# Optimization experiments

Hardware: AMD Instinct MI355X
Metric: run time of the kernel (lower is better)

## Reference

```python
import jax, jax.numpy as jnp
import numpy as np

HC, WC = 248, 224          # coarse grid
HF, WF = 496, 448
C, UNITS = 128, 256
U = UNITS // 4             # combination='concat' -> per-quadrant units


def _build_edges():
    """Upsampling edges: each fine node connects to its unique coarse parent.
    Quadrant split follows the original rel_pos conditions
    [(-0.5,0.5),(0.5,0.5),(0.5,-0.5),(-0.5,-0.5)] == (row,col) parity
    (even,odd),(odd,odd),(odd,even),(even,even)."""
    n_coarse = HC * WC
    rr, cc = np.meshgrid(np.arange(HF), np.arange(WF), indexing='ij')
    parent = (rr // 2) * WC + cc // 2                 # sender = coarse node id
    recv = n_coarse + rr * WF + cc                    # receiver = offset fine node id
    re, ce = rr % 2, cc % 2
    masks = [(re == 0) & (ce == 1), (re == 1) & (ce == 1),
             (re == 1) & (ce == 0), (re == 0) & (ce == 0)]
    return np.stack([np.stack([parent[m], recv[m]], -1) for m in masks]).astype(np.int32)


def setup_inputs() -> dict:
    key = jax.random.key(0)
    k = jax.random.split(key, 4)
    n_coarse = HC * WC
    return {
        'x': jax.random.normal(k[0], (n_coarse, C), jnp.float32),
        'W_emb': jax.random.normal(k[1], (4, C, U), jnp.float32) * 0.05,
        'W_edge': jax.random.normal(k[2], (4, 2 + 2 * U, U), jnp.float32) * 0.05,
        'W_node': jax.random.normal(k[3], (C + 4 * U, UNITS), jnp.float32) * 0.05,
        'edge_idx': jnp.asarray(_build_edges()),   # [4, E, 2] int32
    }


def reference(x, W_emb, W_edge, W_node, edge_idx):
    n_coarse = x.shape[0]
    n_fine = edge_idx.shape[0] * edge_idx.shape[1]
    n_total = n_coarse + n_fine
    # x = concat(old nodes, zeros for new upsampled nodes)
    x_full = jnp.concatenate([x, jnp.zeros((n_fine, x.shape[1]), x.dtype)], axis=0)
    scale = jnp.asarray(1.0 / 4.0, x.dtype)  # 1 / (max_neighbors + 1)
    aggs = []
    for q in range(4):  # 4 structurally distinct quadrant GCNs
        xq = jax.nn.relu(x_full @ W_emb[q])                       # [N_total, U]
        e = edge_idx[q]                                           # [E, 2]
        sender = xq[e[:, 0]]
        receiver = xq[e[:, 1]]
        efeat = jnp.zeros((e.shape[0], 2), xq.dtype)              # edges = zeros_like(edge_index)
        edge = jax.nn.relu(jnp.concatenate([efeat, sender, receiver], -1) @ W_edge[q])
        agg = jax.ops.segment_sum(edge, e[:, 1], num_segments=n_total) * scale
        aggs.append(agg)
    quad_neighbors = jnp.concatenate(aggs, axis=-1)               # [N_total, 4U]
    out = jax.nn.relu(jnp.concatenate([x_full, quad_neighbors], -1) @ W_node)
    return out[n_coarse:]                                         # upsampled fine nodes
```

## Files before the change

### kernel.cpp

```cpp
#include <hip/hip_runtime.h>


typedef __attribute__((ext_vector_type(8))) short bf16x8;
typedef __attribute__((ext_vector_type(4))) float f32x4;
typedef __attribute__((ext_vector_type(4))) unsigned int u32x4;

#define WCOARSE 224
#define WFINE   448
#define NCOARSE 55552

__device__ __forceinline__ unsigned int f2bf(float f) {
    unsigned int u = __builtin_bit_cast(unsigned int, f);
    return (u + 0x7FFFu + ((u >> 16) & 1u)) >> 16;
}
__device__ __forceinline__ unsigned int pk2(float a, float b) {
    return f2bf(a) | (f2bf(b) << 16);
}

__global__ void build_frags(const float* __restrict__ W_emb,
                            const float* __restrict__ W_edge,
                            const float* __restrict__ W_node,
                            unsigned short* __restrict__ ws) {
    int i = blockIdx.x * 256 + threadIdx.x;
    float val;
    if (i < 32768) {
        int v = i & 7, lane = (i >> 3) & 63, frag = (i >> 9) & 15, q = i >> 13;
        int ri = frag >> 2, kt = frag & 3;
        int hf = ri * 16 + (lane & 15);
        int k  = kt * 32 + (lane >> 4) * 8 + v;
        val = W_emb[(q * 128 + k) * 64 + hf];
    } else if (i < 49152) {
        int j = i - 32768;
        int v = j & 7, lane = (j >> 3) & 63, frag = (j >> 9) & 7, q = j >> 12;
        int ri = frag >> 1, kt = frag & 1;
        int ef = ri * 16 + (lane & 15);
        int hf = kt * 32 + (lane >> 4) * 8 + v;
        val = 0.25f * W_edge[(q * 130 + 2 + hf) * 64 + ef];
    } else {
        int j = i - 49152;
        int v = j & 7, lane = (j >> 3) & 63, frag = (j >> 9) & 31, q = j >> 14;
        int tt = frag >> 1, kt = frag & 1;
        int f  = tt * 16 + (lane & 15);
        int ef = kt * 32 + (lane >> 4) * 8 + v;
        val = W_node[(128 + 64 * q + ef) * 256 + f];
    }
    ws[i] = (unsigned short)f2bf(val);
}

__global__ __launch_bounds__(256) void upsample_mfma(
    const float* __restrict__ x,
    const unsigned short* __restrict__ wsf,
    float* __restrict__ out) {

    __shared__ unsigned short lds[4][2][32 * 64];

    const int t    = threadIdx.x;
    const int wave = t >> 6;
    const int lane = t & 63;
    const int c    = lane & 15;
    const int g    = lane >> 4;
    const int q    = wave;
    const int p0   = blockIdx.x * 32;

    const unsigned short* A1 = wsf + q * (16 * 512);
    const unsigned short* A2 = wsf + 32768 + q * (8 * 512);
    const unsigned short* A3 = wsf + 49152 + q * (32 * 512);
    unsigned short* Hb = &lds[wave][0][0];
    unsigned short* Eb = &lds[wave][1][0];

    bf16x8 B1[2][4];
#pragma unroll
    for (int nj = 0; nj < 2; ++nj) {
        const float* xr = x + (p0 + nj * 16 + c) * 128 + g * 8;
#pragma unroll
        for (int kt = 0; kt < 4; ++kt) {
            const float4 a = *reinterpret_cast<const float4*>(xr + kt * 32);
            const float4 b = *reinterpret_cast<const float4*>(xr + kt * 32 + 4);
            u32x4 wv = { pk2(a.x, a.y), pk2(a.z, a.w), pk2(b.x, b.y), pk2(b.z, b.w) };
            B1[nj][kt] = __builtin_bit_cast(bf16x8, wv);
        }
    }
    f32x4 c1[4][2] = {};
#pragma unroll
    for (int kt = 0; kt < 4; ++kt)
#pragma unroll
        for (int ri = 0; ri < 4; ++ri) {
            bf16x8 a = *reinterpret_cast<const bf16x8*>(A1 + ((ri * 4 + kt) * 64 + lane) * 8);
#pragma unroll
            for (int nj = 0; nj < 2; ++nj)
                c1[ri][nj] = __builtin_amdgcn_mfma_f32_16x16x32_bf16(a, B1[nj][kt], c1[ri][nj], 0, 0, 0);
        }
#pragma unroll
    for (int ri = 0; ri < 4; ++ri)
#pragma unroll
        for (int nj = 0; nj < 2; ++nj) {
            const int m = nj * 16 + c;
            const int b = ri * 2 + (g >> 1);
            f32x4 v = c1[ri][nj];
            uint2 w;
            w.x = pk2(fmaxf(v[0], 0.f), fmaxf(v[1], 0.f));
            w.y = pk2(fmaxf(v[2], 0.f), fmaxf(v[3], 0.f));
            *reinterpret_cast<uint2*>(Hb + m * 64 + (((b ^ (m & 7)) << 3) | ((g & 1) << 2))) = w;
        }

    bf16x8 B2[2][2];
#pragma unroll
    for (int nj = 0; nj < 2; ++nj) {
        const int m = nj * 16 + c;
#pragma unroll
        for (int kt = 0; kt < 2; ++kt)
            B2[nj][kt] = *reinterpret_cast<const bf16x8*>(Hb + m * 64 + (((kt * 4 + g) ^ (m & 7)) << 3));
    }
    f32x4 c2[4][2] = {};
#pragma unroll
    for (int kt = 0; kt < 2; ++kt)
#pragma unroll
        for (int ri = 0; ri < 4; ++ri) {
            bf16x8 a = *reinterpret_cast<const bf16x8*>(A2 + ((ri * 2 + kt) * 64 + lane) * 8);
#pragma unroll
            for (int nj = 0; nj < 2; ++nj)
                c2[ri][nj] = __builtin_amdgcn_mfma_f32_16x16x32_bf16(a, B2[nj][kt], c2[ri][nj], 0, 0, 0);
        }
#pragma unroll
    for (int ri = 0; ri < 4; ++ri)
#pragma unroll
        for (int nj = 0; nj < 2; ++nj) {
            const int m = nj * 16 + c;
            const int b = ri * 2 + (g >> 1);
            f32x4 v = c2[ri][nj];
            uint2 w;
            w.x = pk2(fmaxf(v[0], 0.f), fmaxf(v[1], 0.f));
            w.y = pk2(fmaxf(v[2], 0.f), fmaxf(v[3], 0.f));
            *reinterpret_cast<uint2*>(Eb + m * 64 + (((b ^ (m & 7)) << 3) | ((g & 1) << 2))) = w;
        }

    bf16x8 B3[2][2];
#pragma unroll
    for (int nj = 0; nj < 2; ++nj) {
        const int m = nj * 16 + c;
#pragma unroll
        for (int kt = 0; kt < 2; ++kt)
            B3[nj][kt] = *reinterpret_cast<const bf16x8*>(Eb + m * 64 + (((kt * 4 + g) ^ (m & 7)) << 3));
    }
    const int dr = (q == 1 || q == 2) ? 1 : 0;
    const int dc = (q == 0 || q == 1) ? 1 : 0;
    int fbase[2];
#pragma unroll
    for (int nj = 0; nj < 2; ++nj) {
        const int p  = p0 + nj * 16 + c;
        const int pr = p / WCOARSE;
        const int pc = p - pr * WCOARSE;
        fbase[nj] = ((2 * pr + dr) * WFINE + 2 * pc + dc) * 256;
    }
#pragma unroll 4
    for (int tt = 0; tt < 16; ++tt) {
        bf16x8 a0 = *reinterpret_cast<const bf16x8*>(A3 + ((tt * 2 + 0) * 64 + lane) * 8);
        bf16x8 a1 = *reinterpret_cast<const bf16x8*>(A3 + ((tt * 2 + 1) * 64 + lane) * 8);
#pragma unroll
        for (int nj = 0; nj < 2; ++nj) {
            f32x4 o = {};
            o = __builtin_amdgcn_mfma_f32_16x16x32_bf16(a0, B3[nj][0], o, 0, 0, 0);
            o = __builtin_amdgcn_mfma_f32_16x16x32_bf16(a1, B3[nj][1], o, 0, 0, 0);
            float4 s;
            s.x = fmaxf(o[0], 0.f);
            s.y = fmaxf(o[1], 0.f);
            s.z = fmaxf(o[2], 0.f);
            s.w = fmaxf(o[3], 0.f);
            *reinterpret_cast<float4*>(out + fbase[nj] + tt * 16 + g * 4) = s;
        }
    }
}

extern "C" void kernel_launch(void* const* d_in, const int* in_sizes, int n_in,
                              void* d_out, int out_size, void* d_ws, size_t ws_size,
                              hipStream_t stream) {
    const float* x      = (const float*)d_in[0];
    const float* W_emb  = (const float*)d_in[1];
    const float* W_edge = (const float*)d_in[2];
    const float* W_node = (const float*)d_in[3];
    unsigned short* ws  = (unsigned short*)d_ws;
    float* out          = (float*)d_out;

    build_frags<<<448, 256, 0, stream>>>(W_emb, W_edge, W_node, ws);
    upsample_mfma<<<1736, 256, 0, stream>>>(x, ws, out);
}
```

Baseline: 277.3 us.

## Share bf16 x tile via LDS, use hardware bf16 pack, nontemporal output stores

The input tile is now loaded and converted to bf16 once per block into shared memory, instead of each of the four waves reading and converting the same x rows. Manual bf16 rounding is replaced with the v_cvt_pk_bf16_f32 instruction. The H and E buffers now share one fragment-ordered LDS region per wave, which drops the XOR swizzle. Output stores become nontemporal, and launch bounds request three blocks per CU. The cost is an added __syncthreads, and the reused LDS buffer depends on correct intra-wave ordering.

```diff
diff --git a/kernel.cpp b/kernel.cpp
--- a/kernel.cpp
+++ b/kernel.cpp
@@ -13,8 +13,11 @@
     unsigned int u = __builtin_bit_cast(unsigned int, f);
     return (u + 0x7FFFu + ((u >> 16) & 1u)) >> 16;
 }
-__device__ __forceinline__ unsigned int pk2(float a, float b) {
-    return f2bf(a) | (f2bf(b) << 16);
+
+__device__ __forceinline__ unsigned int cvtpk(float lo, float hi) {
+    unsigned int r;
+    asm("v_cvt_pk_bf16_f32 %0, %1, %2" : "=v"(r) : "v"(lo), "v"(hi));
+    return r;
 }
 
 __global__ void build_frags(const float* __restrict__ W_emb,
@@ -47,12 +50,13 @@
     ws[i] = (unsigned short)f2bf(val);
 }
 
-__global__ __launch_bounds__(256) void upsample_mfma(
+__global__ __launch_bounds__(256, 3) void upsample_mfma(
     const float* __restrict__ x,
     const unsigned short* __restrict__ wsf,
     float* __restrict__ out) {
 
-    __shared__ unsigned short lds[4][2][32 * 64];
+    __shared__ unsigned int Xb[2048];
+    __shared__ unsigned int HEb[4][1024];
 
     const int t    = threadIdx.x;
     const int wave = t >> 6;
@@ -62,24 +66,35 @@
     const int q    = wave;
     const int p0   = blockIdx.x * 32;
 
+#pragma unroll
+    for (int half = 0; half < 2; ++half) {
+        const int u  = t * 8 + half * 4;
+        const int g4 = u >> 2;
+        const int ln = g4 & 63;
+        const int kt = (g4 >> 6) & 3;
+        const int nj = g4 >> 8;
+        const int node = nj * 16 + (ln & 15);
+        const int kb   = kt * 32 + (ln >> 4) * 8;
+        const float* src = x + (size_t)(p0 + node) * 128 + kb;
+        const float4 a = *reinterpret_cast<const float4*>(src);
+        const float4 b = *reinterpret_cast<const float4*>(src + 4);
+        u32x4 w = { cvtpk(a.x, a.y), cvtpk(a.z, a.w), cvtpk(b.x, b.y), cvtpk(b.z, b.w) };
+        *reinterpret_cast<u32x4*>(&Xb[u]) = w;
+    }
+    __syncthreads();
+
     const unsigned short* A1 = wsf + q * (16 * 512);
     const unsigned short* A2 = wsf + 32768 + q * (8 * 512);
     const unsigned short* A3 = wsf + 49152 + q * (32 * 512);
-    unsigned short* Hb = &lds[wave][0][0];
-    unsigned short* Eb = &lds[wave][1][0];
+    unsigned int* HE = HEb[wave];
 
     bf16x8 B1[2][4];
 #pragma unroll
-    for (int nj = 0; nj < 2; ++nj) {
-        const float* xr = x + (p0 + nj * 16 + c) * 128 + g * 8;
+    for (int nj = 0; nj < 2; ++nj)
 #pragma unroll
-        for (int kt = 0; kt < 4; ++kt) {
-            const float4 a = *reinterpret_cast<const float4*>(xr + kt * 32);
-            const float4 b = *reinterpret_cast<const float4*>(xr + kt * 32 + 4);
-            u32x4 wv = { pk2(a.x, a.y), pk2(a.z, a.w), pk2(b.x, b.y), pk2(b.z, b.w) };
-            B1[nj][kt] = __builtin_bit_cast(bf16x8, wv);
-        }
-    }
+        for (int kt = 0; kt < 4; ++kt)
+            B1[nj][kt] = *reinterpret_cast<const bf16x8*>(&Xb[((nj * 4 + kt) * 64 + lane) * 4]);
+
     f32x4 c1[4][2] = {};
 #pragma unroll
     for (int kt = 0; kt < 4; ++kt)
@@ -94,23 +109,21 @@
     for (int ri = 0; ri < 4; ++ri)
 #pragma unroll
         for (int nj = 0; nj < 2; ++nj) {
-            const int m = nj * 16 + c;
-            const int b = ri * 2 + (g >> 1);
             f32x4 v = c1[ri][nj];
             uint2 w;
-            w.x = pk2(fmaxf(v[0], 0.f), fmaxf(v[1], 0.f));
-            w.y = pk2(fmaxf(v[2], 0.f), fmaxf(v[3], 0.f));
-            *reinterpret_cast<uint2*>(Hb + m * 64 + (((b ^ (m & 7)) << 3) | ((g & 1) << 2))) = w;
+            w.x = cvtpk(fmaxf(v[0], 0.f), fmaxf(v[1], 0.f));
+            w.y = cvtpk(fmaxf(v[2], 0.f), fmaxf(v[3], 0.f));
+            const int gt = (2 * ri + (g >> 1)) & 3;
+            *reinterpret_cast<uint2*>(&HE[((nj * 2 + (ri >> 1)) * 64 + gt * 16 + c) * 4 + (g & 1) * 2]) = w;
         }
 
     bf16x8 B2[2][2];
 #pragma unroll
-    for (int nj = 0; nj < 2; ++nj) {
-        const int m = nj * 16 + c;
+    for (int nj = 0; nj < 2; ++nj)
 #pragma unroll
         for (int kt = 0; kt < 2; ++kt)
-            B2[nj][kt] = *reinterpret_cast<const bf16x8*>(Hb + m * 64 + (((kt * 4 + g) ^ (m & 7)) << 3));
-    }
+            B2[nj][kt] = *reinterpret_cast<const bf16x8*>(&HE[((nj * 2 + kt) * 64 + lane) * 4]);
+
     f32x4 c2[4][2] = {};
 #pragma unroll
     for (int kt = 0; kt < 2; ++kt)
@@ -125,33 +138,30 @@
     for (int ri = 0; ri < 4; ++ri)
 #pragma unroll
         for (int nj = 0; nj < 2; ++nj) {
-            const int m = nj * 16 + c;
-            const int b = ri * 2 + (g >> 1);
             f32x4 v = c2[ri][nj];
             uint2 w;
-            w.x = pk2(fmaxf(v[0], 0.f), fmaxf(v[1], 0.f));
-            w.y = pk2(fmaxf(v[2], 0.f), fmaxf(v[3], 0.f));
-            *reinterpret_cast<uint2*>(Eb + m * 64 + (((b ^ (m & 7)) << 3) | ((g & 1) << 2))) = w;
+            w.x = cvtpk(fmaxf(v[0], 0.f), fmaxf(v[1], 0.f));
+            w.y = cvtpk(fmaxf(v[2], 0.f), fmaxf(v[3], 0.f));
+            const int gt = (2 * ri + (g >> 1)) & 3;
+            *reinterpret_cast<uint2*>(&HE[((nj * 2 + (ri >> 1)) * 64 + gt * 16 + c) * 4 + (g & 1) * 2]) = w;
         }
 
     bf16x8 B3[2][2];
 #pragma unroll
-    for (int nj = 0; nj < 2; ++nj) {
-        const int m = nj * 16 + c;
+    for (int nj = 0; nj < 2; ++nj)
 #pragma unroll
         for (int kt = 0; kt < 2; ++kt)
-            B3[nj][kt] = *reinterpret_cast<const bf16x8*>(Eb + m * 64 + (((kt * 4 + g) ^ (m & 7)) << 3));
-    }
-    const int dr = (q == 1 || q == 2) ? 1 : 0;
-    const int dc = (q == 0 || q == 1) ? 1 : 0;
-    int fbase[2];
+            B3[nj][kt] = *reinterpret_cast<const bf16x8*>(&HE[((nj * 2 + kt) * 64 + lane) * 4]);
+
+    const int dr  = (q == 1 || q == 2) ? 1 : 0;
+    const int dc  = (q == 0 || q == 1) ? 1 : 0;
+    const int pr  = p0 / WCOARSE;
+    const int pc0 = p0 - pr * WCOARSE;
+    int fb[2];
 #pragma unroll
-    for (int nj = 0; nj < 2; ++nj) {
-        const int p  = p0 + nj * 16 + c;
-        const int pr = p / WCOARSE;
-        const int pc = p - pr * WCOARSE;
-        fbase[nj] = ((2 * pr + dr) * WFINE + 2 * pc + dc) * 256;
-    }
+    for (int nj = 0; nj < 2; ++nj)
+        fb[nj] = ((2 * pr + dr) * WFINE + 2 * (pc0 + nj * 16 + c) + dc) * 256;
+
 #pragma unroll 4
     for (int tt = 0; tt < 16; ++tt) {
         bf16x8 a0 = *reinterpret_cast<const bf16x8*>(A3 + ((tt * 2 + 0) * 64 + lane) * 8);
@@ -161,12 +171,12 @@
             f32x4 o = {};
             o = __builtin_amdgcn_mfma_f32_16x16x32_bf16(a0, B3[nj][0], o, 0, 0, 0);
             o = __builtin_amdgcn_mfma_f32_16x16x32_bf16(a1, B3[nj][1], o, 0, 0, 0);
-            float4 s;
-            s.x = fmaxf(o[0], 0.f);
-            s.y = fmaxf(o[1], 0.f);
-            s.z = fmaxf(o[2], 0.f);
-            s.w = fmaxf(o[3], 0.f);
-            *reinterpret_cast<float4*>(out + fbase[nj] + tt * 16 + g * 4) = s;
+            f32x4 s;
+            s[0] = fmaxf(o[0], 0.f);
+            s[1] = fmaxf(o[1], 0.f);
+            s[2] = fmaxf(o[2], 0.f);
+            s[3] = fmaxf(o[3], 0.f);
+            __builtin_nontemporal_store(s, reinterpret_cast<f32x4*>(out + fb[nj] + tt * 16 + g * 4));
         }
     }
 }
```

Result: slower. 295.4 us (+6.5%).
